# Performance work log

Hardware: AMD Instinct MI355X
Metric: run time of the kernel (lower is better)

## Reference

```python
import jax, jax.numpy as jnp
import numpy as np

V = 33279   # num_tokens
E = 256     # embedding_size
H = 512     # hidden_size
NH = 8      # num_heads
L = 4       # num_layers
DH = E // NH
MAXPOS = 64


def _ln(x, g, b):
    mu = jnp.mean(x, axis=-1, keepdims=True)
    var = jnp.mean((x - mu) ** 2, axis=-1, keepdims=True)
    return (x - mu) / jnp.sqrt(var + 1e-5) * g + b


def setup_inputs() -> dict:
    key = jax.random.key(0)
    ks = jax.random.split(key, 32)
    N, S = 128, 64
    label = jax.random.randint(ks[0], (N, S), 0, V)
    # Bernoulli(0.15) BERT-style mask (deterministic stand-in for torch sampling)
    mask = (jax.random.uniform(ks[1], (N, S)) < 0.15).astype(jnp.int32)
    s = 0.02
    inp = {
        'label': label, 'mask': mask,
        'emb': jax.random.normal(ks[2], (V + 1, E)) * s,
        'pos': jax.random.normal(ks[3], (MAXPOS, E)) * s,
        'emb_g': jnp.ones((E,)), 'emb_b': jnp.zeros((E,)),
        # stacked per-layer params (leading dim L)
        'Wq': jax.random.normal(ks[4], (L, E, E)) * s, 'bq': jnp.zeros((L, E)),
        'Wk': jax.random.normal(ks[5], (L, E, E)) * s, 'bk': jnp.zeros((L, E)),
        'Wv': jax.random.normal(ks[6], (L, E, E)) * s, 'bv': jnp.zeros((L, E)),
        'Wo': jax.random.normal(ks[7], (L, E, E)) * s, 'bo': jnp.zeros((L, E)),
        'n1g': jnp.ones((L, E)), 'n1b': jnp.zeros((L, E)),
        'W1': jax.random.normal(ks[8], (L, E, H)) * s, 'b1': jnp.zeros((L, H)),
        'W2': jax.random.normal(ks[9], (L, H, E)) * s, 'b2': jnp.zeros((L, E)),
        'n2g': jnp.ones((L, E)), 'n2b': jnp.zeros((L, E)),
        # decoder head
        'dW1': jax.random.normal(ks[10], (E, E)) * s, 'db1': jnp.zeros((E,)),
        'dng': jnp.ones((E,)), 'dnb': jnp.zeros((E,)),
        'dW2': jax.random.normal(ks[11], (E, V)) * s, 'db2': jnp.zeros((V,)),
    }
    return inp


def reference(label, mask, emb, pos, emb_g, emb_b, Wq, bq, Wk, bk, Wv, bv,
              Wo, bo, n1g, n1b, W1, b1, W2, b2, n2g, n2b,
              dW1, db1, dng, dnb, dW2, db2):
    N, S = label.shape
    src_ids = jnp.where(mask == 1, V, label)  # masked-token id = num_tokens
    # embedding + positional, then LayerNorm (eval: Scaler/Dropout identity)
    x = emb[src_ids] + pos[:S][None, :, :]
    x = _ln(x, emb_g, emb_b)
    temp = jnp.asarray((E // NH) ** 0.5, x.dtype)

    def layer(x, p):
        wq, bq_, wk, bk_, wv, bv_, wo, bo_, g1, b1n, w1, b1_, w2, b2_, g2, b2n = p
        q = (x @ wq + bq_).reshape(N, S, NH, DH).transpose(0, 2, 1, 3)
        k = (x @ wk + bk_).reshape(N, S, NH, DH).transpose(0, 2, 1, 3)
        v = (x @ wv + bv_).reshape(N, S, NH, DH).transpose(0, 2, 1, 3)
        scores = jnp.einsum('nhsd,nhtd->nhst', q, k) / temp
        attn = jax.nn.softmax(scores, axis=-1)
        o = jnp.einsum('nhst,nhtd->nhsd', attn, v)
        o = o.transpose(0, 2, 1, 3).reshape(N, S, E) @ wo + bo_
        x1 = _ln(x + o, g1, b1n)
        ff = jax.nn.gelu(x1 @ w1 + b1_, approximate=False) @ w2 + b2_
        x2 = _ln(x1 + ff, g2, b2n)
        return x2, None

    x, _ = jax.lax.scan(layer, x, (Wq, bq, Wk, bk, Wv, bv, Wo, bo,
                                   n1g, n1b, W1, b1, W2, b2, n2g, n2b))
    # decoder head: linear -> gelu -> LN -> vocab projection
    h = jax.nn.gelu(x @ dW1 + db1, approximate=False)
    h = _ln(h, dng, dnb)
    logits = h @ dW2 + db2               # [N, S, V]
    logp = jax.nn.log_softmax(logits, axis=-1)
    loss = -jnp.take_along_axis(logp, label[..., None], axis=-1).mean()
    score = logits.transpose(0, 2, 1)    # [N, V, S] like torch permute(0,2,1)
    return score, loss
```

## Files before the change

kernel.cpp:

```cpp
#include <hip/hip_runtime.h>
#include <hip/hip_bf16.h>

#define DEVFN static __device__ __forceinline__
#define MFMA16(a, b, c) __builtin_amdgcn_mfma_f32_16x16x32_bf16((a), (b), (c), 0, 0, 0)

constexpr int N_ = 128, S_ = 64, T_ = N_ * S_;
constexpr int E_ = 256, H_ = 512, NH_ = 8, DH_ = 32, L_ = 4;
constexpr int V_ = 33279, VPAD_ = 33280, NVT_ = VPAD_ / 256;

typedef __attribute__((ext_vector_type(8))) short bf16x8;
typedef __attribute__((ext_vector_type(4))) float f32x4;
typedef unsigned short ushort_t;

DEVFN ushort_t f2bf(float f) {
  unsigned int u = __float_as_uint(f);
  unsigned int r = (u + 0x7fffu + ((u >> 16) & 1u)) >> 16;
  return (ushort_t)r;
}
DEVFN float bf2f(ushort_t u) { return __uint_as_float(((unsigned)u) << 16); }

DEVFN float geluf(float x) {
  return 0.5f * x * (1.f + erff(x * 0.70710678118654752440f));
}

DEVFN float wave_sum(float v) {
  #pragma unroll
  for (int off = 32; off >= 1; off >>= 1) v += __shfl_xor(v, off, 64);
  return v;
}

DEVFN float l15_sum(float v) {
  v += __shfl_xor(v, 1, 64);
  v += __shfl_xor(v, 2, 64);
  v += __shfl_xor(v, 4, 64);
  v += __shfl_xor(v, 8, 64);
  return v;
}

__global__ __launch_bounds__(256) void k_embed_ln(
    const int* __restrict__ label, const int* __restrict__ mask,
    const float* __restrict__ emb, const float* __restrict__ pos,
    const float* __restrict__ g, const float* __restrict__ b,
    float* __restrict__ x, ushort_t* __restrict__ xb) {
  int wv = threadIdx.x >> 6, lane = threadIdx.x & 63;
  int t = blockIdx.x * 4 + wv;
  int s = t & (S_ - 1);
  int id = (mask[t] == 1) ? V_ : label[t];
  int c = lane * 4;
  float4 v = *(const float4*)&emb[(size_t)id * E_ + c];
  float4 p = *(const float4*)&pos[s * E_ + c];
  v.x += p.x; v.y += p.y; v.z += p.z; v.w += p.w;
  float mean = wave_sum(v.x + v.y + v.z + v.w) * (1.f / E_);
  float4 d = {v.x - mean, v.y - mean, v.z - mean, v.w - mean};
  float var = wave_sum(d.x * d.x + d.y * d.y + d.z * d.z + d.w * d.w) * (1.f / E_);
  float rstd = 1.f / sqrtf(var + 1e-5f);
  float4 g4 = *(const float4*)&g[c];
  float4 b4 = *(const float4*)&b[c];
  float4 y = {d.x * rstd * g4.x + b4.x, d.y * rstd * g4.y + b4.y,
              d.z * rstd * g4.z + b4.z, d.w * rstd * g4.w + b4.w};
  *(float4*)&x[(size_t)t * E_ + c] = y;
  ushort4 yb = {f2bf(y.x), f2bf(y.y), f2bf(y.z), f2bf(y.w)};
  *(ushort4*)&xb[(size_t)t * E_ + c] = yb;
}

__global__ __launch_bounds__(256) void k_prep(
    const float* __restrict__ Wq, const float* __restrict__ Wk,
    const float* __restrict__ Wv, const float* __restrict__ Wo,
    const float* __restrict__ dW1, const float* __restrict__ W1,
    const float* __restrict__ W2, const float* __restrict__ bq,
    const float* __restrict__ bk, const float* __restrict__ bv,
    ushort_t* __restrict__ wqkvT, ushort_t* __restrict__ woT,
    ushort_t* __restrict__ dw1T, ushort_t* __restrict__ w1T,
    ushort_t* __restrict__ w2T, float* __restrict__ bqkv) {
  int z = blockIdx.z;
  if (z == 25) {
    if (blockIdx.x == 0 && blockIdx.y == 0) {
      for (int i = threadIdx.x; i < L_ * 768; i += 256) {
        int l = i / 768, c = i - l * 768;
        float v = (c < 256) ? bq[l * 256 + c]
                : (c < 512) ? bk[l * 256 + c - 256]
                            : bv[l * 256 + c - 512];
        bqkv[i] = v;
      }
    }
    return;
  }
  const float* src;
  ushort_t* dst;
  int K, J;
  if (z < 17) {
    if (blockIdx.x >= 8 || blockIdx.y >= 8) return;
    K = 256; J = 256;
    if (z == 16) { src = dW1; dst = dw1T; }
    else {
      int w = z >> 2, l = z & 3;
      const float* ws = (w == 0) ? Wq : (w == 1) ? Wk : (w == 2) ? Wv : Wo;
      src = ws + (size_t)l * 65536;
      dst = (w < 3) ? (wqkvT + (size_t)l * 768 * 256 + (size_t)w * 256 * 256)
                    : (woT + (size_t)l * 65536);
    }
  } else if (z < 21) {
    int l = z - 17; K = 256; J = 512;
    if (blockIdx.y >= 8) return;
    src = W1 + (size_t)l * K * J; dst = w1T + (size_t)l * J * K;
  } else {
    int l = z - 21; K = 512; J = 256;
    if (blockIdx.x >= 8) return;
    src = W2 + (size_t)l * K * J; dst = w2T + (size_t)l * J * K;
  }
  __shared__ float tile[32][33];
  int j0 = blockIdx.x * 32, k0 = blockIdx.y * 32;
  int tx = threadIdx.x & 31, ty = threadIdx.x >> 5;
  #pragma unroll
  for (int rr = 0; rr < 4; rr++) {
    int kk = ty * 4 + rr;
    tile[kk][tx] = src[(size_t)(k0 + kk) * J + j0 + tx];
  }
  __syncthreads();
  #pragma unroll
  for (int rr = 0; rr < 4; rr++) {
    int jj = ty * 4 + rr;
    dst[(size_t)(j0 + jj) * K + k0 + tx] = f2bf(tile[tx][jj]);
  }
}

__global__ __launch_bounds__(256) void k_qa(
    const ushort_t* __restrict__ xb, const ushort_t* __restrict__ wqkvT_l,
    const float* __restrict__ bqkv_l, ushort_t* __restrict__ o) {
  __shared__ __align__(16) ushort_t xs[64 * 264];
  __shared__ __align__(16) ushort_t qs[64 * 40];
  __shared__ __align__(16) ushort_t ks[64 * 40];
  __shared__ __align__(16) ushort_t vt_[32 * 72];
  int n = blockIdx.x >> 3, h = blockIdx.x & 7;
  int tid = threadIdx.x, lane = tid & 63, wv = tid >> 6;
  int l15 = lane & 15, l4 = lane >> 4;
  const ushort_t* xsrc = xb + (size_t)n * S_ * E_;
  for (int i = tid; i < 64 * 32; i += 256) {
    int r = i >> 5, c = (i & 31) * 8;
    *(uint4*)&xs[r * 264 + c] = *(const uint4*)&xsrc[(size_t)r * E_ + c];
  }
  __syncthreads();
  const ushort_t* xrow = &xs[(wv * 16 + l15) * 264 + l4 * 8];
  const ushort_t* wq = wqkvT_l + (size_t)(h * 32) * E_ + l4 * 8;
  const ushort_t* wk = wqkvT_l + (size_t)(256 + h * 32) * E_ + l4 * 8;
  const ushort_t* wvp = wqkvT_l + (size_t)(512 + h * 32) * E_ + l4 * 8;
  f32x4 qa[2] = {}, ka[2] = {}, va[2] = {};
  #pragma unroll
  for (int kb = 0; kb < 8; kb++) {
    bf16x8 a = *(const bf16x8*)(xrow + kb * 32);
    #pragma unroll
    for (int st = 0; st < 2; st++) {
      bf16x8 bq_ = *(const bf16x8*)(wq + (size_t)(st * 16 + l15) * E_ + kb * 32);
      bf16x8 bk_ = *(const bf16x8*)(wk + (size_t)(st * 16 + l15) * E_ + kb * 32);
      bf16x8 bv_ = *(const bf16x8*)(wvp + (size_t)(st * 16 + l15) * E_ + kb * 32);
      qa[st] = MFMA16(a, bq_, qa[st]);
      ka[st] = MFMA16(a, bk_, ka[st]);
      va[st] = MFMA16(a, bv_, va[st]);
    }
  }
  #pragma unroll
  for (int st = 0; st < 2; st++) {
    int c = st * 16 + l15;
    float bqv = bqkv_l[h * 32 + c];
    float bkv = bqkv_l[256 + h * 32 + c];
    float bvv = bqkv_l[512 + h * 32 + c];
    #pragma unroll
    for (int r = 0; r < 4; r++) {
      int t = wv * 16 + l4 * 4 + r;
      qs[t * 40 + c] = f2bf(qa[st][r] + bqv);
      ks[t * 40 + c] = f2bf(ka[st][r] + bkv);
      vt_[c * 72 + t] = f2bf(va[st][r] + bvv);
    }
  }
  __syncthreads();
  int srow = wv * 16 + l15;
  bf16x8 aq = *(const bf16x8*)&qs[srow * 40 + l4 * 8];
  f32x4 sc[4];
  #pragma unroll
  for (int st = 0; st < 4; st++) {
    bf16x8 bk_ = *(const bf16x8*)&ks[(st * 16 + l15) * 40 + l4 * 8];
    f32x4 z = {};
    sc[st] = MFMA16(aq, bk_, z);
  }
  const float scale = 0.17677669529663687f;
  #pragma unroll
  for (int st = 0; st < 4; st++)
    #pragma unroll
    for (int r = 0; r < 4; r++) sc[st][r] *= scale;
  ushort_t* ps = xs;
  #pragma unroll
  for (int r = 0; r < 4; r++) {
    float m = fmaxf(fmaxf(sc[0][r], sc[1][r]), fmaxf(sc[2][r], sc[3][r]));
    m = fmaxf(m, __shfl_xor(m, 1, 64));
    m = fmaxf(m, __shfl_xor(m, 2, 64));
    m = fmaxf(m, __shfl_xor(m, 4, 64));
    m = fmaxf(m, __shfl_xor(m, 8, 64));
    float p0 = __expf(sc[0][r] - m), p1 = __expf(sc[1][r] - m);
    float p2 = __expf(sc[2][r] - m), p3 = __expf(sc[3][r] - m);
    float sum = p0 + p1 + p2 + p3;
    sum += __shfl_xor(sum, 1, 64);
    sum += __shfl_xor(sum, 2, 64);
    sum += __shfl_xor(sum, 4, 64);
    sum += __shfl_xor(sum, 8, 64);
    float inv = 1.f / sum;
    int prow = (wv * 16 + l4 * 4 + r) * 72;
    ps[prow + 0 * 16 + l15] = f2bf(p0 * inv);
    ps[prow + 1 * 16 + l15] = f2bf(p1 * inv);
    ps[prow + 2 * 16 + l15] = f2bf(p2 * inv);
    ps[prow + 3 * 16 + l15] = f2bf(p3 * inv);
  }
  f32x4 oc[2] = {};
  #pragma unroll
  for (int kb = 0; kb < 2; kb++) {
    bf16x8 ap = *(const bf16x8*)&ps[srow * 72 + kb * 32 + l4 * 8];
    #pragma unroll
    for (int st2 = 0; st2 < 2; st2++) {
      bf16x8 bv_ = *(const bf16x8*)&vt_[(st2 * 16 + l15) * 72 + kb * 32 + l4 * 8];
      oc[st2] = MFMA16(ap, bv_, oc[st2]);
    }
  }
  ushort_t* ob = o + (size_t)n * S_ * E_ + h * DH_;
  #pragma unroll
  for (int st2 = 0; st2 < 2; st2++)
    #pragma unroll
    for (int r = 0; r < 4; r++)
      ob[(size_t)(wv * 16 + l4 * 4 + r) * E_ + st2 * 16 + l15] = f2bf(oc[st2][r]);
}

template <int K, int GELU_PRE>
__global__ __launch_bounds__(256) void k_mm_ln2(
    const ushort_t* __restrict__ Xb, const ushort_t* __restrict__ WT,
    const float* __restrict__ bias, const float* __restrict__ g,
    const float* __restrict__ bet, ushort_t* __restrict__ yb) {
  constexpr int STR = K + 8;
  __shared__ ushort_t xs[16 * STR];
  __shared__ float redA[4][16], redB[4][16];
  int tid = threadIdx.x, lane = tid & 63, wv = tid >> 6;
  int t0 = blockIdx.x * 16;
  const ushort_t* xsrc = Xb + (size_t)t0 * K;
  for (int i = tid; i < 16 * (K / 8); i += 256) {
    int r = i / (K / 8), c = (i % (K / 8)) * 8;
    *(uint4*)&xs[r * STR + c] = *(const uint4*)&xsrc[(size_t)r * K + c];
  }
  __syncthreads();
  int l15 = lane & 15, l4 = lane >> 4;
  f32x4 acc[4] = {};
  const ushort_t* xrow = &xs[l15 * STR + l4 * 8];
  const ushort_t* wrow = WT + (size_t)(wv * 64) * K + l4 * 8;
  #pragma unroll
  for (int kb = 0; kb < K / 32; kb++) {
    bf16x8 a = *(const bf16x8*)(xrow + kb * 32);
    #pragma unroll
    for (int st = 0; st < 4; st++) {
      bf16x8 bfr = *(const bf16x8*)(wrow + (size_t)(st * 16 + l15) * K + kb * 32);
      acc[st] = MFMA16(a, bfr, acc[st]);
    }
  }
  float val[4][4];
  #pragma unroll
  for (int st = 0; st < 4; st++) {
    int j = wv * 64 + st * 16 + l15;
    float bv_ = bias[j];
    #pragma unroll
    for (int r = 0; r < 4; r++) {
      float v = acc[st][r] + bv_;
      if (GELU_PRE) v = geluf(v);
      val[st][r] = v;
    }
  }
  #pragma unroll
  for (int r = 0; r < 4; r++) {
    float s = val[0][r] + val[1][r] + val[2][r] + val[3][r];
    s = l15_sum(s);
    if (l15 == 0) redA[wv][l4 * 4 + r] = s;
  }
  __syncthreads();
  float mean[4];
  #pragma unroll
  for (int r = 0; r < 4; r++) {
    int row = l4 * 4 + r;
    mean[r] = (redA[0][row] + redA[1][row] + redA[2][row] + redA[3][row]) * (1.f / E_);
  }
  #pragma unroll
  for (int r = 0; r < 4; r++) {
    float s = 0.f;
    #pragma unroll
    for (int st = 0; st < 4; st++) {
      float d = val[st][r] - mean[r];
      s += d * d;
    }
    s = l15_sum(s);
    if (l15 == 0) redB[wv][l4 * 4 + r] = s;
  }
  __syncthreads();
  float rstd[4];
  #pragma unroll
  for (int r = 0; r < 4; r++) {
    int row = l4 * 4 + r;
    float var = (redB[0][row] + redB[1][row] + redB[2][row] + redB[3][row]) * (1.f / E_);
    rstd[r] = 1.f / sqrtf(var + 1e-5f);
  }
  #pragma unroll
  for (int st = 0; st < 4; st++) {
    int j = wv * 64 + st * 16 + l15;
    float gj = g[j], bj = bet[j];
    #pragma unroll
    for (int r = 0; r < 4; r++) {
      int t = t0 + l4 * 4 + r;
      yb[(size_t)t * E_ + j] = f2bf((val[st][r] - mean[r]) * rstd[r] * gj + bj);
    }
  }
}

__global__ __launch_bounds__(256) void k_aof(
    const ushort_t* __restrict__ obuf, const ushort_t* __restrict__ woT_l,
    const float* __restrict__ bo_l, const float* __restrict__ xres,
    const float* __restrict__ g1, const float* __restrict__ b1n,
    const ushort_t* __restrict__ w1T_l, const float* __restrict__ b1v,
    const ushort_t* __restrict__ w2T_l, const float* __restrict__ b2v,
    const float* __restrict__ g2, const float* __restrict__ b2n,
    float* __restrict__ yout, ushort_t* __restrict__ ybout) {
  __shared__ ushort_t xs[16 * 264];
  __shared__ ushort_t hsd[16 * 520];
  __shared__ float redA[4][16], redB[4][16];
  int tid = threadIdx.x, lane = tid & 63, wv = tid >> 6;
  int t0 = blockIdx.x * 16;
  int l15 = lane & 15, l4 = lane >> 4;
  const ushort_t* osrc = obuf + (size_t)t0 * E_;
  for (int i = tid; i < 16 * 32; i += 256) {
    int r = i >> 5, c = (i & 31) * 8;
    *(uint4*)&xs[r * 264 + c] = *(const uint4*)&osrc[(size_t)r * E_ + c];
  }
  __syncthreads();
  f32x4 acc[4] = {};
  {
    const ushort_t* xrow = &xs[l15 * 264 + l4 * 8];
    const ushort_t* wrow = woT_l + (size_t)(wv * 64) * E_ + l4 * 8;
    #pragma unroll
    for (int kb = 0; kb < 8; kb++) {
      bf16x8 a = *(const bf16x8*)(xrow + kb * 32);
      #pragma unroll
      for (int st = 0; st < 4; st++) {
        bf16x8 b = *(const bf16x8*)(wrow + (size_t)(st * 16 + l15) * E_ + kb * 32);
        acc[st] = MFMA16(a, b, acc[st]);
      }
    }
  }
  float val[4][4];
  #pragma unroll
  for (int st = 0; st < 4; st++) {
    int j = wv * 64 + st * 16 + l15;
    float bv_ = bo_l[j];
    #pragma unroll
    for (int r = 0; r < 4; r++)
      val[st][r] = acc[st][r] + bv_ + xres[(size_t)(t0 + l4 * 4 + r) * E_ + j];
  }
  #pragma unroll
  for (int r = 0; r < 4; r++) {
    float s = l15_sum(val[0][r] + val[1][r] + val[2][r] + val[3][r]);
    if (l15 == 0) redA[wv][l4 * 4 + r] = s;
  }
  __syncthreads();
  float mean[4];
  #pragma unroll
  for (int r = 0; r < 4; r++) {
    int row = l4 * 4 + r;
    mean[r] = (redA[0][row] + redA[1][row] + redA[2][row] + redA[3][row]) * (1.f / E_);
  }
  #pragma unroll
  for (int r = 0; r < 4; r++) {
    float s = 0.f;
    #pragma unroll
    for (int st = 0; st < 4; st++) {
      float d = val[st][r] - mean[r];
      s += d * d;
    }
    s = l15_sum(s);
    if (l15 == 0) redB[wv][l4 * 4 + r] = s;
  }
  __syncthreads();
  #pragma unroll
  for (int r = 0; r < 4; r++) {
    int row = l4 * 4 + r;
    float var = (redB[0][row] + redB[1][row] + redB[2][row] + redB[3][row]) * (1.f / E_);
    float rstd = 1.f / sqrtf(var + 1e-5f);
    #pragma unroll
    for (int st = 0; st < 4; st++) {
      int j = wv * 64 + st * 16 + l15;
      val[st][r] = (val[st][r] - mean[r]) * rstd * g1[j] + b1n[j];
    }
  }
  #pragma unroll
  for (int st = 0; st < 4; st++) {
    int j = wv * 64 + st * 16 + l15;
    #pragma unroll
    for (int r = 0; r < 4; r++)
      xs[(l4 * 4 + r) * 264 + j] = f2bf(val[st][r]);
  }
  __syncthreads();
  f32x4 acc1[8] = {};
  {
    const ushort_t* xrow = &xs[l15 * 264 + l4 * 8];
    const ushort_t* w1r = w1T_l + (size_t)(wv * 128) * E_ + l4 * 8;
    #pragma unroll
    for (int kb = 0; kb < 8; kb++) {
      bf16x8 a = *(const bf16x8*)(xrow + kb * 32);
      #pragma unroll
      for (int ht = 0; ht < 8; ht++) {
        bf16x8 b = *(const bf16x8*)(w1r + (size_t)(ht * 16 + l15) * E_ + kb * 32);
        acc1[ht] = MFMA16(a, b, acc1[ht]);
      }
    }
  }
  #pragma unroll
  for (int ht = 0; ht < 8; ht++) {
    int hc = wv * 128 + ht * 16 + l15;
    float bv_ = b1v[hc];
    #pragma unroll
    for (int r = 0; r < 4; r++)
      hsd[(l4 * 4 + r) * 520 + hc] = f2bf(geluf(acc1[ht][r] + bv_));
  }
  __syncthreads();
  f32x4 acc2[4] = {};
  {
    const ushort_t* hrow = &hsd[l15 * 520 + l4 * 8];
    const ushort_t* w2r = w2T_l + (size_t)(wv * 64) * H_ + l4 * 8;
    #pragma unroll
    for (int kb = 0; kb < 16; kb++) {
      bf16x8 a = *(const bf16x8*)(hrow + kb * 32);
      #pragma unroll
      for (int st = 0; st < 4; st++) {
        bf16x8 b = *(const bf16x8*)(w2r + (size_t)(st * 16 + l15) * H_ + kb * 32);
        acc2[st] = MFMA16(a, b, acc2[st]);
      }
    }
  }
  #pragma unroll
  for (int st = 0; st < 4; st++) {
    int j = wv * 64 + st * 16 + l15;
    float bv_ = b2v[j];
    #pragma unroll
    for (int r = 0; r < 4; r++)
      val[st][r] += acc2[st][r] + bv_;
  }
  #pragma unroll
  for (int r = 0; r < 4; r++) {
    float s = l15_sum(val[0][r] + val[1][r] + val[2][r] + val[3][r]);
    if (l15 == 0) redA[wv][l4 * 4 + r] = s;
  }
  __syncthreads();
  #pragma unroll
  for (int r = 0; r < 4; r++) {
    int row = l4 * 4 + r;
    mean[r] = (redA[0][row] + redA[1][row] + redA[2][row] + redA[3][row]) * (1.f / E_);
  }
  #pragma unroll
  for (int r = 0; r < 4; r++) {
    float s = 0.f;
    #pragma unroll
    for (int st = 0; st < 4; st++) {
      float d = val[st][r] - mean[r];
      s += d * d;
    }
    s = l15_sum(s);
    if (l15 == 0) redB[wv][l4 * 4 + r] = s;
  }
  __syncthreads();
  #pragma unroll
  for (int r = 0; r < 4; r++) {
    int row = l4 * 4 + r;
    float var = (redB[0][row] + redB[1][row] + redB[2][row] + redB[3][row]) * (1.f / E_);
    float rstd = 1.f / sqrtf(var + 1e-5f);
    int t = t0 + l4 * 4 + r;
    #pragma unroll
    for (int st = 0; st < 4; st++) {
      int j = wv * 64 + st * 16 + l15;
      float o = (val[st][r] - mean[r]) * rstd * g2[j] + b2n[j];
      if (yout) yout[(size_t)t * E_ + j] = o;
      ybout[(size_t)t * E_ + j] = f2bf(o);
    }
  }
}

__global__ __launch_bounds__(256) void k_w2t(const float* __restrict__ w,
                                             ushort_t* __restrict__ wt) {
  __shared__ float tile[32 * 33];
  int tx = threadIdx.x & 31, ty = threadIdx.x >> 5;
  int v0 = blockIdx.x * 32, k0 = blockIdx.y * 32;
  #pragma unroll
  for (int rr = 0; rr < 4; rr++) {
    int kk = ty * 4 + rr;
    int vv = v0 + tx;
    tile[kk * 33 + tx] = (vv < V_) ? w[(size_t)(k0 + kk) * V_ + vv] : 0.f;
  }
  __syncthreads();
  #pragma unroll
  for (int rr = 0; rr < 4; rr++) {
    int vv = ty * 4 + rr;
    wt[(size_t)(v0 + vv) * E_ + k0 + tx] = f2bf(tile[tx * 33 + vv]);
  }
}

__global__ __launch_bounds__(256) void k_vocab(
    const ushort_t* __restrict__ hbf, const ushort_t* __restrict__ wt,
    const float* __restrict__ db2, float* __restrict__ out,
    float* __restrict__ pmax, float* __restrict__ psum) {
  __shared__ ushort_t hs[64 * 264];
  __shared__ float redm[4][64];
  __shared__ float reds[4][64];
  int n = blockIdx.x, vt = blockIdx.y;
  int tid = threadIdx.x, lane = tid & 63, wv = tid >> 6;
  const ushort_t* hsrc = hbf + (size_t)n * S_ * E_;
  for (int i = tid; i < (S_ * E_) / 8; i += 256) {
    int s = i >> 5, kc = (i & 31) * 8;
    *(uint4*)&hs[s * 264 + kc] = *(const uint4*)&hsrc[s * E_ + kc];
  }
  __syncthreads();
  int l15 = lane & 15, l4 = lane >> 4;
  float rm[4], rs[4];
  #pragma unroll
  for (int st = 0; st < 4; st++) { rm[st] = -INFINITY; rs[st] = 0.f; }
  #pragma unroll
  for (int h2 = 0; h2 < 2; h2++) {
    const ushort_t* Ap0 =
        wt + (size_t)(vt * 256 + h2 * 128 + wv * 16 + l15) * E_ + l4 * 8;
    const ushort_t* Ap1 = Ap0 + (size_t)64 * E_;
    f32x4 acc[2][4] = {};
    #pragma unroll
    for (int kb = 0; kb < 8; kb++) {
      bf16x8 a0 = *(const bf16x8*)(Ap0 + kb * 32);
      bf16x8 a1 = *(const bf16x8*)(Ap1 + kb * 32);
      #pragma unroll
      for (int st = 0; st < 4; st++) {
        bf16x8 bfr = *(const bf16x8*)&hs[(st * 16 + l15) * 264 + kb * 32 + l4 * 8];
        acc[0][st] = MFMA16(a0, bfr, acc[0][st]);
        acc[1][st] = MFMA16(a1, bfr, acc[1][st]);
      }
    }
    float vals[2][4][4];
    #pragma unroll
    for (int mt = 0; mt < 2; mt++) {
      #pragma unroll
      for (int j = 0; j < 4; j++) {
        int v = vt * 256 + h2 * 128 + wv * 16 + mt * 64 + l4 * 4 + j;
        bool valid = v < V_;
        float bias = valid ? db2[v] : 0.f;
        size_t ob = ((size_t)n * V_ + v) * S_;
        #pragma unroll
        for (int st = 0; st < 4; st++) {
          float val = valid ? (acc[mt][st][j] + bias) : -INFINITY;
          vals[mt][st][j] = val;
          if (valid) __builtin_nontemporal_store(val, &out[ob + st * 16 + l15]);
        }
      }
    }
    #pragma unroll
    for (int st = 0; st < 4; st++) {
      float m = -INFINITY;
      #pragma unroll
      for (int mt = 0; mt < 2; mt++)
        #pragma unroll
        for (int j = 0; j < 4; j++) m = fmaxf(m, vals[mt][st][j]);
      m = fmaxf(m, __shfl_xor(m, 16, 64));
      m = fmaxf(m, __shfl_xor(m, 32, 64));
      float sum = 0.f;
      #pragma unroll
      for (int mt = 0; mt < 2; mt++)
        #pragma unroll
        for (int j = 0; j < 4; j++) sum += __expf(vals[mt][st][j] - m);
      sum += __shfl_xor(sum, 16, 64);
      sum += __shfl_xor(sum, 32, 64);
      float nm = fmaxf(rm[st], m);
      rs[st] = rs[st] * __expf(rm[st] - nm) + sum * __expf(m - nm);
      rm[st] = nm;
    }
  }
  if (l4 == 0) {
    #pragma unroll
    for (int st = 0; st < 4; st++) {
      redm[wv][st * 16 + l15] = rm[st];
      reds[wv][st * 16 + l15] = rs[st];
    }
  }
  __syncthreads();
  if (wv == 0 && l4 == 0) {
    #pragma unroll
    for (int st = 0; st < 4; st++) {
      int s = st * 16 + l15;
      float M = fmaxf(fmaxf(redm[0][s], redm[1][s]), fmaxf(redm[2][s], redm[3][s]));
      float Sa = reds[0][s] * __expf(redm[0][s] - M) +
                 reds[1][s] * __expf(redm[1][s] - M) +
                 reds[2][s] * __expf(redm[2][s] - M) +
                 reds[3][s] * __expf(redm[3][s] - M);
      size_t pi = ((size_t)n * NVT_ + vt) * S_ + s;
      pmax[pi] = M;
      psum[pi] = Sa;
    }
  }
}

__global__ __launch_bounds__(512) void k_lossf(
    const float* __restrict__ pmax, const float* __restrict__ psum,
    const float* __restrict__ out, const int* __restrict__ label,
    float* __restrict__ partial) {
  __shared__ float sm[512], ssum[512];
  int n = blockIdx.x, tid = threadIdx.x;
  int s = tid & 63, qq = tid >> 6;
  float m = -INFINITY, sum = 0.f;
  for (int vt = qq; vt < NVT_; vt += 8) {
    size_t pi = ((size_t)n * NVT_ + vt) * S_ + s;
    float m2 = pmax[pi], s2 = psum[pi];
    float nm = fmaxf(m, m2);
    sum = sum * __expf(m - nm) + s2 * __expf(m2 - nm);
    m = nm;
  }
  sm[tid] = m; ssum[tid] = sum;
  __syncthreads();
  if (qq == 0) {
    float M = sm[s], Sa = ssum[s];
    #pragma unroll
    for (int p = 1; p < 8; p++) {
      float m2 = sm[p * 64 + s], s2 = ssum[p * 64 + s];
      float nm = fmaxf(M, m2);
      Sa = Sa * __expf(M - nm) + s2 * __expf(m2 - nm);
      M = nm;
    }
    float lse = M + logf(Sa);
    int lab = label[n * S_ + s];
    float lx = out[((size_t)n * V_ + lab) * S_ + s];
    partial[n * S_ + s] = lse - lx;
  }
}

__global__ __launch_bounds__(256) void k_loss2(const float* __restrict__ partial,
                                               float* __restrict__ dst) {
  __shared__ float sbuf[4];
  int tid = threadIdx.x;
  float acc = 0.f;
  for (int i = tid; i < T_; i += 256) acc += partial[i];
  #pragma unroll
  for (int off = 32; off >= 1; off >>= 1) acc += __shfl_xor(acc, off, 64);
  int lane = tid & 63, wid = tid >> 6;
  if (lane == 0) sbuf[wid] = acc;
  __syncthreads();
  if (tid == 0) dst[0] = (sbuf[0] + sbuf[1] + sbuf[2] + sbuf[3]) / (float)T_;
}

extern "C" void kernel_launch(void* const* d_in, const int* in_sizes, int n_in,
                              void* d_out, int out_size, void* d_ws, size_t ws_size,
                              hipStream_t stream) {
  const int*   label = (const int*)d_in[0];
  const int*   mask  = (const int*)d_in[1];
  const float* emb   = (const float*)d_in[2];
  const float* pos   = (const float*)d_in[3];
  const float* emb_g = (const float*)d_in[4];
  const float* emb_b = (const float*)d_in[5];
  const float* Wq  = (const float*)d_in[6];
  const float* bq  = (const float*)d_in[7];
  const float* Wk  = (const float*)d_in[8];
  const float* bk  = (const float*)d_in[9];
  const float* Wv  = (const float*)d_in[10];
  const float* bv  = (const float*)d_in[11];
  const float* Wo  = (const float*)d_in[12];
  const float* bo  = (const float*)d_in[13];
  const float* n1g = (const float*)d_in[14];
  const float* n1b = (const float*)d_in[15];
  const float* W1  = (const float*)d_in[16];
  const float* b1  = (const float*)d_in[17];
  const float* W2  = (const float*)d_in[18];
  const float* b2  = (const float*)d_in[19];
  const float* n2g = (const float*)d_in[20];
  const float* n2b = (const float*)d_in[21];
  const float* dW1 = (const float*)d_in[22];
  const float* db1 = (const float*)d_in[23];
  const float* dng = (const float*)d_in[24];
  const float* dnb = (const float*)d_in[25];
  const float* dW2 = (const float*)d_in[26];
  const float* db2 = (const float*)d_in[27];
  float* out = (float*)d_out;
  (void)in_sizes; (void)n_in; (void)out_size; (void)ws_size;

  char* base = (char*)d_ws;
  size_t off = 0;
  auto alloc = [&](size_t bytes) {
    char* p = base + off;
    off += (bytes + 255) & ~(size_t)255;
    return p;
  };
  float*    x    = (float*)alloc((size_t)T_ * E_ * 4);
  ushort_t* xb   = (ushort_t*)alloc((size_t)T_ * E_ * 2);
  ushort_t* obuf = (ushort_t*)alloc((size_t)T_ * E_ * 2);
  ushort_t* wqkvT = (ushort_t*)alloc((size_t)L_ * 768 * E_ * 2);
  ushort_t* woT   = (ushort_t*)alloc((size_t)L_ * E_ * E_ * 2);
  ushort_t* w1T   = (ushort_t*)alloc((size_t)L_ * H_ * E_ * 2);
  ushort_t* w2T   = (ushort_t*)alloc((size_t)L_ * E_ * H_ * 2);
  ushort_t* dw1T  = (ushort_t*)alloc((size_t)E_ * E_ * 2);
  ushort_t* wt    = (ushort_t*)alloc((size_t)VPAD_ * E_ * 2);
  float*    bqkv  = (float*)alloc((size_t)L_ * 768 * 4);
  float*    partial = (float*)alloc((size_t)T_ * 4);
  ushort_t* hbf = obuf;
  float* pmax = x;
  float* psum = pmax + (size_t)N_ * NVT_ * S_;

  k_prep<<<dim3(16, 16, 26), 256, 0, stream>>>(Wq, Wk, Wv, Wo, dW1, W1, W2,
                                               bq, bk, bv, wqkvT, woT, dw1T,
                                               w1T, w2T, bqkv);
  k_w2t<<<dim3(VPAD_ / 32, E_ / 32), 256, 0, stream>>>(dW2, wt);

  k_embed_ln<<<T_ / 4, 256, 0, stream>>>(label, mask, emb, pos, emb_g, emb_b, x, xb);

  for (int l = 0; l < L_; l++) {
    k_qa<<<N_ * NH_, 256, 0, stream>>>(
        xb, wqkvT + (size_t)l * 768 * E_, bqkv + l * 768, obuf);
    k_aof<<<T_ / 16, 256, 0, stream>>>(
        obuf, woT + (size_t)l * E_ * E_, bo + l * E_, x,
        n1g + l * E_, n1b + l * E_,
        w1T + (size_t)l * H_ * E_, b1 + l * H_,
        w2T + (size_t)l * E_ * H_, b2 + l * E_,
        n2g + l * E_, n2b + l * E_,
        (l == L_ - 1) ? nullptr : x, xb);
  }

  k_mm_ln2<E_, 1><<<T_ / 16, 256, 0, stream>>>(xb, dw1T, db1, dng, dnb, hbf);

  k_vocab<<<dim3(N_, NVT_), 256, 0, stream>>>(hbf, wt, db2, out, pmax, psum);

  k_lossf<<<N_, 512, 0, stream>>>(pmax, psum, out, label, partial);
  k_loss2<<<1, 256, 0, stream>>>(partial, out + (size_t)N_ * V_ * S_);
}
```

Baseline: 809.5 us.

## Fuse decoder head into last layer and restructure vocab projection epilogue

The last encoder-layer kernel becomes a template variant that keeps the normalized output in shared memory and runs the decoder dense+GELU+LayerNorm in place, removing the separate k_mm_ln2 launch and one activation round trip. The vocab kernel swaps MFMA operand roles so each wave owns 16 sequence positions and sweeps 256 vocab rows. This lets it issue vectorized float4 nontemporal logit stores and do the softmax partial reduction with in-register shuffles, with no shared-memory cross-wave merge. The partial max and sum are packed into float2, and the loss-finalize kernel uses 1024 threads. In exchange, every wave now re-reads the full vocab weight tile, so weight traffic per block is four times higher, relying on cache hits.

Result: slower. 1.400 ms (+72.9%).

```diff
diff --git a/kernel.cpp b/kernel.cpp
--- a/kernel.cpp
+++ b/kernel.cpp
@@ -34,6 +34,14 @@
   v += __shfl_xor(v, 2, 64);
   v += __shfl_xor(v, 4, 64);
   v += __shfl_xor(v, 8, 64);
+  return v;
+}
+
+DEVFN float l15_max(float v) {
+  v = fmaxf(v, __shfl_xor(v, 1, 64));
+  v = fmaxf(v, __shfl_xor(v, 2, 64));
+  v = fmaxf(v, __shfl_xor(v, 4, 64));
+  v = fmaxf(v, __shfl_xor(v, 8, 64));
   return v;
 }
 
@@ -227,91 +235,7 @@
       ob[(size_t)(wv * 16 + l4 * 4 + r) * E_ + st2 * 16 + l15] = f2bf(oc[st2][r]);
 }
 
-template <int K, int GELU_PRE>
-__global__ __launch_bounds__(256) void k_mm_ln2(
-    const ushort_t* __restrict__ Xb, const ushort_t* __restrict__ WT,
-    const float* __restrict__ bias, const float* __restrict__ g,
-    const float* __restrict__ bet, ushort_t* __restrict__ yb) {
-  constexpr int STR = K + 8;
-  __shared__ ushort_t xs[16 * STR];
-  __shared__ float redA[4][16], redB[4][16];
-  int tid = threadIdx.x, lane = tid & 63, wv = tid >> 6;
-  int t0 = blockIdx.x * 16;
-  const ushort_t* xsrc = Xb + (size_t)t0 * K;
-  for (int i = tid; i < 16 * (K / 8); i += 256) {
-    int r = i / (K / 8), c = (i % (K / 8)) * 8;
-    *(uint4*)&xs[r * STR + c] = *(const uint4*)&xsrc[(size_t)r * K + c];
-  }
-  __syncthreads();
-  int l15 = lane & 15, l4 = lane >> 4;
-  f32x4 acc[4] = {};
-  const ushort_t* xrow = &xs[l15 * STR + l4 * 8];
-  const ushort_t* wrow = WT + (size_t)(wv * 64) * K + l4 * 8;
-  #pragma unroll
-  for (int kb = 0; kb < K / 32; kb++) {
-    bf16x8 a = *(const bf16x8*)(xrow + kb * 32);
-    #pragma unroll
-    for (int st = 0; st < 4; st++) {
-      bf16x8 bfr = *(const bf16x8*)(wrow + (size_t)(st * 16 + l15) * K + kb * 32);
-      acc[st] = MFMA16(a, bfr, acc[st]);
-    }
-  }
-  float val[4][4];
-  #pragma unroll
-  for (int st = 0; st < 4; st++) {
-    int j = wv * 64 + st * 16 + l15;
-    float bv_ = bias[j];
-    #pragma unroll
-    for (int r = 0; r < 4; r++) {
-      float v = acc[st][r] + bv_;
-      if (GELU_PRE) v = geluf(v);
-      val[st][r] = v;
-    }
-  }
-  #pragma unroll
-  for (int r = 0; r < 4; r++) {
-    float s = val[0][r] + val[1][r] + val[2][r] + val[3][r];
-    s = l15_sum(s);
-    if (l15 == 0) redA[wv][l4 * 4 + r] = s;
-  }
-  __syncthreads();
-  float mean[4];
-  #pragma unroll
-  for (int r = 0; r < 4; r++) {
-    int row = l4 * 4 + r;
-    mean[r] = (redA[0][row] + redA[1][row] + redA[2][row] + redA[3][row]) * (1.f / E_);
-  }
-  #pragma unroll
-  for (int r = 0; r < 4; r++) {
-    float s = 0.f;
-    #pragma unroll
-    for (int st = 0; st < 4; st++) {
-      float d = val[st][r] - mean[r];
-      s += d * d;
-    }
-    s = l15_sum(s);
-    if (l15 == 0) redB[wv][l4 * 4 + r] = s;
-  }
-  __syncthreads();
-  float rstd[4];
-  #pragma unroll
-  for (int r = 0; r < 4; r++) {
-    int row = l4 * 4 + r;
-    float var = (redB[0][row] + redB[1][row] + redB[2][row] + redB[3][row]) * (1.f / E_);
-    rstd[r] = 1.f / sqrtf(var + 1e-5f);
-  }
-  #pragma unroll
-  for (int st = 0; st < 4; st++) {
-    int j = wv * 64 + st * 16 + l15;
-    float gj = g[j], bj = bet[j];
-    #pragma unroll
-    for (int r = 0; r < 4; r++) {
-      int t = t0 + l4 * 4 + r;
-      yb[(size_t)t * E_ + j] = f2bf((val[st][r] - mean[r]) * rstd[r] * gj + bj);
-    }
-  }
-}
-
+template <int LAST>
 __global__ __launch_bounds__(256) void k_aof(
     const ushort_t* __restrict__ obuf, const ushort_t* __restrict__ woT_l,
     const float* __restrict__ bo_l, const float* __restrict__ xres,
@@ -319,7 +243,10 @@
     const ushort_t* __restrict__ w1T_l, const float* __restrict__ b1v,
     const ushort_t* __restrict__ w2T_l, const float* __restrict__ b2v,
     const float* __restrict__ g2, const float* __restrict__ b2n,
-    float* __restrict__ yout, ushort_t* __restrict__ ybout) {
+    float* __restrict__ yout, ushort_t* __restrict__ ybout,
+    const ushort_t* __restrict__ dw1T, const float* __restrict__ db1h,
+    const float* __restrict__ gH, const float* __restrict__ bH,
+    ushort_t* __restrict__ hbf) {
   __shared__ ushort_t xs[16 * 264];
   __shared__ ushort_t hsd[16 * 520];
   __shared__ float redA[4][16], redB[4][16];
@@ -466,18 +393,91 @@
     if (l15 == 0) redB[wv][l4 * 4 + r] = s;
   }
   __syncthreads();
-  #pragma unroll
-  for (int r = 0; r < 4; r++) {
-    int row = l4 * 4 + r;
-    float var = (redB[0][row] + redB[1][row] + redB[2][row] + redB[3][row]) * (1.f / E_);
-    float rstd = 1.f / sqrtf(var + 1e-5f);
-    int t = t0 + l4 * 4 + r;
+  if (!LAST) {
+    #pragma unroll
+    for (int r = 0; r < 4; r++) {
+      int row = l4 * 4 + r;
+      float var = (redB[0][row] + redB[1][row] + redB[2][row] + redB[3][row]) * (1.f / E_);
+      float rstd = 1.f / sqrtf(var + 1e-5f);
+      int t = t0 + l4 * 4 + r;
+      #pragma unroll
+      for (int st = 0; st < 4; st++) {
+        int j = wv * 64 + st * 16 + l15;
+        float o = (val[st][r] - mean[r]) * rstd * g2[j] + b2n[j];
+        yout[(size_t)t * E_ + j] = o;
+        ybout[(size_t)t * E_ + j] = f2bf(o);
+      }
+    }
+  } else {
+    #pragma unroll
+    for (int r = 0; r < 4; r++) {
+      int row = l4 * 4 + r;
+      float var = (redB[0][row] + redB[1][row] + redB[2][row] + redB[3][row]) * (1.f / E_);
+      float rstd = 1.f / sqrtf(var + 1e-5f);
+      #pragma unroll
+      for (int st = 0; st < 4; st++) {
+        int j = wv * 64 + st * 16 + l15;
+        float o = (val[st][r] - mean[r]) * rstd * g2[j] + b2n[j];
+        xs[(l4 * 4 + r) * 264 + j] = f2bf(o);
+      }
+    }
+    __syncthreads();
+    f32x4 acch[4] = {};
+    {
+      const ushort_t* xrow = &xs[l15 * 264 + l4 * 8];
+      const ushort_t* wrow = dw1T + (size_t)(wv * 64) * E_ + l4 * 8;
+      #pragma unroll
+      for (int kb = 0; kb < 8; kb++) {
+        bf16x8 a = *(const bf16x8*)(xrow + kb * 32);
+        #pragma unroll
+        for (int st = 0; st < 4; st++) {
+          bf16x8 b = *(const bf16x8*)(wrow + (size_t)(st * 16 + l15) * E_ + kb * 32);
+          acch[st] = MFMA16(a, b, acch[st]);
+        }
+      }
+    }
     #pragma unroll
     for (int st = 0; st < 4; st++) {
       int j = wv * 64 + st * 16 + l15;
-      float o = (val[st][r] - mean[r]) * rstd * g2[j] + b2n[j];
-      if (yout) yout[(size_t)t * E_ + j] = o;
-      ybout[(size_t)t * E_ + j] = f2bf(o);
+      float bv_ = db1h[j];
+      #pragma unroll
+      for (int r = 0; r < 4; r++)
+        val[st][r] = geluf(acch[st][r] + bv_);
+    }
+    #pragma unroll
+    for (int r = 0; r < 4; r++) {
+      float s = l15_sum(val[0][r] + val[1][r] + val[2][r] + val[3][r]);
+      if (l15 == 0) redA[wv][l4 * 4 + r] = s;
+    }
+    __syncthreads();
+    #pragma unroll
+    for (int r = 0; r < 4; r++) {
+      int row = l4 * 4 + r;
+      mean[r] = (redA[0][row] + redA[1][row] + redA[2][row] + redA[3][row]) * (1.f / E_);
+    }
+    #pragma unroll
+    for (int r = 0; r < 4; r++) {
+      float s = 0.f;
+      #pragma unroll
+      for (int st = 0; st < 4; st++) {
+        float d = val[st][r] - mean[r];
+        s += d * d;
+      }
+      s = l15_sum(s);
+      if (l15 == 0) redB[wv][l4 * 4 + r] = s;
+    }
+    __syncthreads();
+    #pragma unroll
+    for (int r = 0; r < 4; r++) {
+      int row = l4 * 4 + r;
+      float var = (redB[0][row] + redB[1][row] + redB[2][row] + redB[3][row]) * (1.f / E_);
+      float rstd = 1.f / sqrtf(var + 1e-5f);
+      int t = t0 + l4 * 4 + r;
+      #pragma unroll
+      for (int st = 0; st < 4; st++) {
+        int j = wv * 64 + st * 16 + l15;
+        hbf[(size_t)t * E_ + j] = f2bf((val[st][r] - mean[r]) * rstd * gH[j] + bH[j]);
+      }
     }
   }
 }
@@ -504,10 +504,8 @@
 __global__ __launch_bounds__(256) void k_vocab(
     const ushort_t* __restrict__ hbf, const ushort_t* __restrict__ wt,
     const float* __restrict__ db2, float* __restrict__ out,
-    float* __restrict__ pmax, float* __restrict__ psum) {
+    float2* __restrict__ psp) {
   __shared__ ushort_t hs[64 * 264];
-  __shared__ float redm[4][64];
-  __shared__ float reds[4][64];
   int n = blockIdx.x, vt = blockIdx.y;
   int tid = threadIdx.x, lane = tid & 63, wv = tid >> 6;
   const ushort_t* hsrc = hbf + (size_t)n * S_ * E_;
@@ -517,101 +515,67 @@
   }
   __syncthreads();
   int l15 = lane & 15, l4 = lane >> 4;
-  float rm[4], rs[4];
-  #pragma unroll
-  for (int st = 0; st < 4; st++) { rm[st] = -INFINITY; rs[st] = 0.f; }
-  #pragma unroll
-  for (int h2 = 0; h2 < 2; h2++) {
-    const ushort_t* Ap0 =
-        wt + (size_t)(vt * 256 + h2 * 128 + wv * 16 + l15) * E_ + l4 * 8;
-    const ushort_t* Ap1 = Ap0 + (size_t)64 * E_;
-    f32x4 acc[2][4] = {};
-    #pragma unroll
-    for (int kb = 0; kb < 8; kb++) {
-      bf16x8 a0 = *(const bf16x8*)(Ap0 + kb * 32);
-      bf16x8 a1 = *(const bf16x8*)(Ap1 + kb * 32);
-      #pragma unroll
-      for (int st = 0; st < 4; st++) {
-        bf16x8 bfr = *(const bf16x8*)&hs[(st * 16 + l15) * 264 + kb * 32 + l4 * 8];
-        acc[0][st] = MFMA16(a0, bfr, acc[0][st]);
-        acc[1][st] = MFMA16(a1, bfr, acc[1][st]);
-      }
-    }
-    float vals[2][4][4];
-    #pragma unroll
-    for (int mt = 0; mt < 2; mt++) {
-      #pragma unroll
-      for (int j = 0; j < 4; j++) {
-        int v = vt * 256 + h2 * 128 + wv * 16 + mt * 64 + l4 * 4 + j;
-        bool valid = v < V_;
-        float bias = valid ? db2[v] : 0.f;
-        size_t ob = ((size_t)n * V_ + v) * S_;
-        #pragma unroll
-        for (int st = 0; st < 4; st++) {
-          float val = valid ? (acc[mt][st][j] + bias) : -INFINITY;
-          vals[mt][st][j] = val;
-          if (valid) __builtin_nontemporal_store(val, &out[ob + st * 16 + l15]);
-        }
-      }
-    }
-    #pragma unroll
-    for (int st = 0; st < 4; st++) {
-      float m = -INFINITY;
-      #pragma unroll
-      for (int mt = 0; mt < 2; mt++)
-        #pragma unroll
-        for (int j = 0; j < 4; j++) m = fmaxf(m, vals[mt][st][j]);
-      m = fmaxf(m, __shfl_xor(m, 16, 64));
-      m = fmaxf(m, __shfl_xor(m, 32, 64));
-      float sum = 0.f;
-      #pragma unroll
-      for (int mt = 0; mt < 2; mt++)
-        #pragma unroll
-        for (int j = 0; j < 4; j++) sum += __expf(vals[mt][st][j] - m);
-      sum += __shfl_xor(sum, 16, 64);
-      sum += __shfl_xor(sum, 32, 64);
-      float nm = fmaxf(rm[st], m);
-      rs[st] = rs[st] * __expf(rm[st] - nm) + sum * __expf(m - nm);
-      rm[st] = nm;
-    }
-  }
-  if (l4 == 0) {
-    #pragma unroll
-    for (int st = 0; st < 4; st++) {
-      redm[wv][st * 16 + l15] = rm[st];
-      reds[wv][st * 16 + l15] = rs[st];
-    }
-  }
-  __syncthreads();
-  if (wv == 0 && l4 == 0) {
-    #pragma unroll
-    for (int st = 0; st < 4; st++) {
-      int s = st * 16 + l15;
-      float M = fmaxf(fmaxf(redm[0][s], redm[1][s]), fmaxf(redm[2][s], redm[3][s]));
-      float Sa = reds[0][s] * __expf(redm[0][s] - M) +
-                 reds[1][s] * __expf(redm[1][s] - M) +
-                 reds[2][s] * __expf(redm[2][s] - M) +
-                 reds[3][s] * __expf(redm[3][s] - M);
-      size_t pi = ((size_t)n * NVT_ + vt) * S_ + s;
-      pmax[pi] = M;
-      psum[pi] = Sa;
-    }
-  }
-}
-
-__global__ __launch_bounds__(512) void k_lossf(
-    const float* __restrict__ pmax, const float* __restrict__ psum,
-    const float* __restrict__ out, const int* __restrict__ label,
-    float* __restrict__ partial) {
-  __shared__ float sm[512], ssum[512];
+  bf16x8 afrag[8];
+  #pragma unroll
+  for (int kb = 0; kb < 8; kb++)
+    afrag[kb] = *(const bf16x8*)&hs[(wv * 16 + l15) * 264 + kb * 32 + l4 * 8];
+  f32x4 acc[16];
+  const ushort_t* wbase = wt + (size_t)(vt * 256 + l15) * E_ + l4 * 8;
+  #pragma unroll
+  for (int v16 = 0; v16 < 16; v16++) {
+    f32x4 a = {};
+    const ushort_t* wr = wbase + (size_t)(v16 * 16) * E_;
+    #pragma unroll
+    for (int kb = 0; kb < 8; kb++)
+      a = MFMA16(afrag[kb], *(const bf16x8*)(wr + kb * 32), a);
+    acc[v16] = a;
+  }
+  int s0 = wv * 16 + l4 * 4;
+  float m[4] = {-INFINITY, -INFINITY, -INFINITY, -INFINITY};
+  #pragma unroll
+  for (int v16 = 0; v16 < 16; v16++) {
+    int v = vt * 256 + v16 * 16 + l15;
+    bool valid = v < V_;
+    float bias = valid ? db2[v] : 0.f;
+    #pragma unroll
+    for (int r = 0; r < 4; r++) {
+      float x = valid ? (acc[v16][r] + bias) : -INFINITY;
+      acc[v16][r] = x;
+      m[r] = fmaxf(m[r], x);
+    }
+    if (valid)
+      __builtin_nontemporal_store(acc[v16],
+                                  (f32x4*)&out[((size_t)n * V_ + v) * S_ + s0]);
+  }
+  #pragma unroll
+  for (int r = 0; r < 4; r++) m[r] = l15_max(m[r]);
+  float sum[4] = {0.f, 0.f, 0.f, 0.f};
+  #pragma unroll
+  for (int v16 = 0; v16 < 16; v16++)
+    #pragma unroll
+    for (int r = 0; r < 4; r++) sum[r] += __expf(acc[v16][r] - m[r]);
+  #pragma unroll
+  for (int r = 0; r < 4; r++) sum[r] = l15_sum(sum[r]);
+  if (l15 == 0) {
+    #pragma unroll
+    for (int r = 0; r < 4; r++) {
+      float2 p = {m[r], sum[r]};
+      psp[((size_t)n * NVT_ + vt) * S_ + s0 + r] = p;
+    }
+  }
+}
+
+__global__ __launch_bounds__(1024) void k_lossf(
+    const float2* __restrict__ psp, const float* __restrict__ out,
+    const int* __restrict__ label, float* __restrict__ partial) {
+  __shared__ float sm[1024], ssum[1024];
   int n = blockIdx.x, tid = threadIdx.x;
   int s = tid & 63, qq = tid >> 6;
   float m = -INFINITY, sum = 0.f;
-  for (int vt = qq; vt < NVT_; vt += 8) {
-    size_t pi = ((size_t)n * NVT_ + vt) * S_ + s;
-    float m2 = pmax[pi], s2 = psum[pi];
-    float nm = fmaxf(m, m2);
-    sum = sum * __expf(m - nm) + s2 * __expf(m2 - nm);
+  for (int vt = qq; vt < NVT_; vt += 16) {
+    float2 p = psp[((size_t)n * NVT_ + vt) * S_ + s];
+    float nm = fmaxf(m, p.x);
+    sum = sum * __expf(m - nm) + p.y * __expf(p.x - nm);
     m = nm;
   }
   sm[tid] = m; ssum[tid] = sum;
@@ -619,7 +583,7 @@
   if (qq == 0) {
     float M = sm[s], Sa = ssum[s];
     #pragma unroll
-    for (int p = 1; p < 8; p++) {
+    for (int p = 1; p < 16; p++) {
       float m2 = sm[p * 64 + s], s2 = ssum[p * 64 + s];
       float nm = fmaxf(M, m2);
       Sa = Sa * __expf(M - nm) + s2 * __expf(m2 - nm);
@@ -699,8 +663,7 @@
   float*    bqkv  = (float*)alloc((size_t)L_ * 768 * 4);
   float*    partial = (float*)alloc((size_t)T_ * 4);
   ushort_t* hbf = obuf;
-  float* pmax = x;
-  float* psum = pmax + (size_t)N_ * NVT_ * S_;
+  float2* psp = (float2*)x;
 
   k_prep<<<dim3(16, 16, 26), 256, 0, stream>>>(Wq, Wk, Wv, Wo, dW1, W1, W2,
                                                bq, bk, bv, wqkvT, woT, dw1T,
@@ -712,19 +675,27 @@
   for (int l = 0; l < L_; l++) {
     k_qa<<<N_ * NH_, 256, 0, stream>>>(
         xb, wqkvT + (size_t)l * 768 * E_, bqkv + l * 768, obuf);
-    k_aof<<<T_ / 16, 256, 0, stream>>>(
-        obuf, woT + (size_t)l * E_ * E_, bo + l * E_, x,
-        n1g + l * E_, n1b + l * E_,
-        w1T + (size_t)l * H_ * E_, b1 + l * H_,
-        w2T + (size_t)l * E_ * H_, b2 + l * E_,
-        n2g + l * E_, n2b + l * E_,
-        (l == L_ - 1) ? nullptr : x, xb);
-  }
-
-  k_mm_ln2<E_, 1><<<T_ / 16, 256, 0, stream>>>(xb, dw1T, db1, dng, dnb, hbf);
-
-  k_vocab<<<dim3(N_, NVT_), 256, 0, stream>>>(hbf, wt, db2, out, pmax, psum);
-
-  k_lossf<<<N_, 512, 0, stream>>>(pmax, psum, out, label, partial);
+    if (l < L_ - 1) {
+      k_aof<0><<<T_ / 16, 256, 0, stream>>>(
+          obuf, woT + (size_t)l * E_ * E_, bo + l * E_, x,
+          n1g + l * E_, n1b + l * E_,
+          w1T + (size_t)l * H_ * E_, b1 + l * H_,
+          w2T + (size_t)l * E_ * H_, b2 + l * E_,
+          n2g + l * E_, n2b + l * E_, x, xb,
+          nullptr, nullptr, nullptr, nullptr, nullptr);
+    } else {
+      k_aof<1><<<T_ / 16, 256, 0, stream>>>(
+          obuf, woT + (size_t)l * E_ * E_, bo + l * E_, x,
+          n1g + l * E_, n1b + l * E_,
+          w1T + (size_t)l * H_ * E_, b1 + l * H_,
+          w2T + (size_t)l * E_ * H_, b2 + l * E_,
+          n2g + l * E_, n2b + l * E_, nullptr, nullptr,
+          dw1T, db1, dng, dnb, hbf);
+    }
+  }
+
+  k_vocab<<<dim3(N_, NVT_), 256, 0, stream>>>(hbf, wt, db2, out, psp);
+
+  k_lossf<<<N_, 1024, 0, stream>>>(psp, out, label, partial);
   k_loss2<<<1, 256, 0, stream>>>(partial, out + (size_t)N_ * V_ * S_);
 }
```
